# Performance work log

Measured on AMD Instinct MI355X. Metric: run time of the kernel, lower is better.

Reference implementation:

```python
import jax, jax.numpy as jnp
import numpy as np

T, B, E, H = 1024, 2, 1024, 16
D = E // H


def setup_inputs() -> dict:
    key = jax.random.key(0)
    ks = jax.random.split(key, 5)
    s = 1.0 / np.sqrt(E)  # xavier_uniform bound ~ sqrt(6/(fan_in+fan_out)); scale suffices for a numeric baseline
    return {
        "query": jax.random.normal(ks[0], (T, B, E), jnp.float32),
        "key_": jax.random.normal(ks[1], (T, B, E), jnp.float32),
        "value": jax.random.normal(ks[2], (T, B, E), jnp.float32),
        "in_proj_weight": jax.random.uniform(ks[3], (3 * E, E), jnp.float32, -s, s),
        "in_proj_bias": jnp.zeros((3 * E,), jnp.float32),
        "out_proj_weight": jax.random.uniform(ks[4], (E, E), jnp.float32, -s, s),
        "out_proj_bias": jnp.zeros((E,), jnp.float32),
    }


def reference(query, key_, value, in_proj_weight, in_proj_bias, out_proj_weight, out_proj_bias):
    # Faithful to CumulativeLinearMultiheadAttentionKV.forward with
    # batch_first=False, is_causal=True, no padding mask, no kv cache.
    Tl, Bl, El = query.shape
    wq, wk, wv = jnp.split(in_proj_weight, 3, axis=0)
    bq, bk, bv = jnp.split(in_proj_bias, 3)
    q = query @ wq.T + bq          # (T, B, E)
    k = key_ @ wk.T + bk
    v = value @ wv.T + bv

    def to_bhtd(x):
        return x.reshape(Tl, Bl, H, D).transpose(1, 2, 0, 3)  # (B, H, T, D)

    q, k, v = to_bhtd(q), to_bhtd(k), to_bhtd(v)

    scale = 1.0 / np.sqrt(D)  # SDPA-style default scale (scale=None)
    # cumulative linear attention: prefix sums of k_s \otimes v_s
    kv = jnp.einsum('bhsk,bhsv->bhskv', k, v)        # (B, H, T, D, D)
    kv_store = jnp.cumsum(kv, axis=2)                # causal KV state per step
    out = jnp.einsum('bhtk,bhtkv->bhtv', q, kv_store) * scale  # (B, H, T, D)

    out = out.transpose(2, 0, 1, 3).reshape(Tl, Bl, El)  # back to (T, B, E)
    out = out @ out_proj_weight.T + out_proj_bias
    return out
```

## Files before the change

kernel.cpp:

```cpp
#include <hip/hip_runtime.h>


#define T_SEQ 1024
#define B_SZ  2
#define E_DIM 1024
#define H_N   16
#define D_HD  64
#define NROWS (T_SEQ * B_SZ)
#define CHUNK 64
#define NCHUNK (T_SEQ / CHUNK)
#define BH (B_SZ * H_N)

typedef short bf16x8 __attribute__((ext_vector_type(8)));
typedef float f32x4  __attribute__((ext_vector_type(4)));

__device__ inline unsigned short f2bf(float f) {
    unsigned u = __builtin_bit_cast(unsigned, f);
    u = (u + 0x7FFFu + ((u >> 16) & 1u)) >> 16;
    return (unsigned short)u;
}

__device__ inline void gload_lds16(const void* g, void* l) {
    __builtin_amdgcn_global_load_lds(
        (const __attribute__((address_space(1))) unsigned int*)g,
        (__attribute__((address_space(3))) unsigned int*)l, 16, 0, 0);
}

__global__ __launch_bounds__(256) void k_castw(
    const float* __restrict__ w_in, const float* __restrict__ w_out,
    unsigned short* __restrict__ dst)
{
    const int id8 = blockIdx.x * 256 + threadIdx.x;
    const int WI8 = 3 * E_DIM * E_DIM / 8;
    const float* src = (id8 < WI8) ? (w_in + (size_t)id8 * 8)
                                   : (w_out + (size_t)(id8 - WI8) * 8);
    float4 f0 = *reinterpret_cast<const float4*>(src);
    float4 f1 = *reinterpret_cast<const float4*>(src + 4);
    ushort4 o0, o1;
    o0.x = f2bf(f0.x); o0.y = f2bf(f0.y); o0.z = f2bf(f0.z); o0.w = f2bf(f0.w);
    o1.x = f2bf(f1.x); o1.y = f2bf(f1.y); o1.z = f2bf(f1.z); o1.w = f2bf(f1.w);
    *reinterpret_cast<ushort4*>(dst + (size_t)id8 * 8)     = o0;
    *reinterpret_cast<ushort4*>(dst + (size_t)id8 * 8 + 4) = o1;
}

__global__ __launch_bounds__(256) void k_gin(
    const float* __restrict__ q_in, const float* __restrict__ k_in,
    const float* __restrict__ v_in, const unsigned short* __restrict__ Wibf,
    const float* __restrict__ b_in,
    unsigned short* __restrict__ qslab, unsigned short* __restrict__ kslab,
    unsigned short* __restrict__ ktb,   unsigned short* __restrict__ vtb)
{
    const int z = blockIdx.z;
    const float* X = (z == 0) ? q_in : (z == 1 ? k_in : v_in);
    const unsigned short* W = Wibf + (size_t)z * E_DIM * E_DIM;
    const float* bz = b_in + z * E_DIM;

    const int nBase = blockIdx.x * 128;
    const int mBase = blockIdx.y * 64;
    const int b = mBase >> 10;
    const int tBase = mBase & 1023;

    __shared__ short As[64 * 72];
    __shared__ short Bs[128 * 64];

    const int tid = threadIdx.x;
    const int lane = tid & 63, wave = tid >> 6;
    const int wr = wave >> 1, wc = wave & 1;
    const int l15 = lane & 15, l4 = lane >> 4;

    f32x4 acc[2][4] = {};

    for (int k0 = 0; k0 < E_DIM; k0 += 64) {
        #pragma unroll
        for (int l = 0; l < 4; ++l) {
            int off = l * 4096 + tid * 16;
            int row = off >> 7, kb = off & 127;
            gload_lds16((const char*)W + ((size_t)(nBase + row) * E_DIM + k0) * 2 + kb,
                        (char*)Bs + off);
        }
        #pragma unroll
        for (int l = 0; l < 2; ++l) {
            int u = tid + 256 * l;
            int row = u >> 3, ko = (u & 7) * 8;
            const float* src = &X[(size_t)((tBase + row) * 2 + b) * E_DIM + k0 + ko];
            float4 f0 = *reinterpret_cast<const float4*>(src);
            float4 f1 = *reinterpret_cast<const float4*>(src + 4);
            bf16x8 p;
            p[0] = (short)f2bf(f0.x); p[1] = (short)f2bf(f0.y);
            p[2] = (short)f2bf(f0.z); p[3] = (short)f2bf(f0.w);
            p[4] = (short)f2bf(f1.x); p[5] = (short)f2bf(f1.y);
            p[6] = (short)f2bf(f1.z); p[7] = (short)f2bf(f1.w);
            *reinterpret_cast<bf16x8*>(&As[row * 72 + ko]) = p;
        }
        __syncthreads();

        #pragma unroll
        for (int kk = 0; kk < 64; kk += 32) {
            bf16x8 af[2], bfr[4];
            #pragma unroll
            for (int i = 0; i < 2; ++i)
                af[i] = *reinterpret_cast<const bf16x8*>(
                            &As[(wr * 32 + i * 16 + l15) * 72 + kk + l4 * 8]);
            #pragma unroll
            for (int j = 0; j < 4; ++j)
                bfr[j] = *reinterpret_cast<const bf16x8*>(
                            &Bs[(wc * 64 + j * 16 + l15) * 64 + kk + l4 * 8]);
            #pragma unroll
            for (int i = 0; i < 2; ++i)
                #pragma unroll
                for (int j = 0; j < 4; ++j)
                    acc[i][j] = __builtin_amdgcn_mfma_f32_16x16x32_bf16(
                        af[i], bfr[j], acc[i][j], 0, 0, 0);
        }
        __syncthreads();
    }

    #pragma unroll
    for (int i = 0; i < 2; ++i) {
        int t0 = tBase + wr * 32 + i * 16 + l4 * 4;
        #pragma unroll
        for (int j = 0; j < 4; ++j) {
            int col = nBase + wc * 64 + j * 16 + l15;
            float bv = bz[col];
            unsigned short v4[4];
            #pragma unroll
            for (int q = 0; q < 4; ++q) v4[q] = f2bf(acc[i][j][q] + bv);
            if (z == 0) {
                #pragma unroll
                for (int q = 0; q < 4; ++q)
                    qslab[(size_t)b * 1048576 + (size_t)(t0 + q) * E_DIM + col] = v4[q];
            } else if (z == 1) {
                #pragma unroll
                for (int q = 0; q < 4; ++q)
                    kslab[(size_t)b * 1048576 + (size_t)(t0 + q) * E_DIM + col] = v4[q];
                ushort4 w = {v4[0], v4[1], v4[2], v4[3]};
                *reinterpret_cast<ushort4*>(
                    &ktb[((size_t)b * 1024 + col) * 1024 + t0]) = w;
            } else {
                ushort4 w = {v4[0], v4[1], v4[2], v4[3]};
                *reinterpret_cast<ushort4*>(
                    &vtb[((size_t)b * 1024 + col) * 1024 + t0]) = w;
            }
        }
    }
}

__global__ __launch_bounds__(256) void k_chunkkv(
    const unsigned short* __restrict__ ktb, const unsigned short* __restrict__ vtb,
    float* __restrict__ ckvT)
{
    const int c = blockIdx.x, bh = blockIdx.y;
    const int b = bh >> 4, h = bh & 15;
    const int colb = h * 64, t0 = c * CHUNK;

    __shared__ short Avs[64 * 64];
    __shared__ short Bks[64 * 64];

    const int tid = threadIdx.x;
    const int lane = tid & 63, wave = tid >> 6;
    const int wr = wave >> 1, wc = wave & 1;
    const int l15 = lane & 15, l4 = lane >> 4;

    #pragma unroll
    for (int l = 0; l < 2; ++l) {
        int off = l * 4096 + tid * 16;
        int row = off >> 7, kb = off & 127;
        size_t rbase = ((size_t)(b * 1024 + colb + row)) * 1024 + t0;
        gload_lds16((const char*)vtb + rbase * 2 + kb, (char*)Avs + off);
        gload_lds16((const char*)ktb + rbase * 2 + kb, (char*)Bks + off);
    }
    __syncthreads();

    f32x4 acc[2][2] = {};
    #pragma unroll
    for (int kk = 0; kk < 64; kk += 32) {
        bf16x8 af[2], bfr[2];
        #pragma unroll
        for (int i = 0; i < 2; ++i)
            af[i] = *reinterpret_cast<const bf16x8*>(
                        &Avs[(wr * 32 + i * 16 + l15) * 64 + kk + l4 * 8]);
        #pragma unroll
        for (int j = 0; j < 2; ++j)
            bfr[j] = *reinterpret_cast<const bf16x8*>(
                        &Bks[(wc * 32 + j * 16 + l15) * 64 + kk + l4 * 8]);
        #pragma unroll
        for (int i = 0; i < 2; ++i)
            #pragma unroll
            for (int j = 0; j < 2; ++j)
                acc[i][j] = __builtin_amdgcn_mfma_f32_16x16x32_bf16(
                    af[i], bfr[j], acc[i][j], 0, 0, 0);
    }

    float* dst = ckvT + ((size_t)bh * NCHUNK + c) * 4096;
    #pragma unroll
    for (int i = 0; i < 2; ++i) {
        int dv = wr * 32 + i * 16 + l4 * 4;
        #pragma unroll
        for (int j = 0; j < 2; ++j) {
            int dk = wc * 32 + j * 16 + l15;
            #pragma unroll
            for (int q = 0; q < 4; ++q)
                dst[(dv + q) * 64 + dk] = acc[i][j][q];
        }
    }
}

__global__ __launch_bounds__(256) void k_prefix(float* __restrict__ ckv)
{
    int id = blockIdx.x * blockDim.x + threadIdx.x;
    int bh = id >> 10, i4 = id & 1023;
    float4 run = {0.f, 0.f, 0.f, 0.f};
    float* base = ckv + (size_t)bh * NCHUNK * 4096 + (size_t)i4 * 4;
    for (int c = 0; c < NCHUNK; ++c) {
        float4* p = reinterpret_cast<float4*>(base + (size_t)c * 4096);
        float4 v = *p;
        *p = run;
        run.x += v.x; run.y += v.y; run.z += v.z; run.w += v.w;
    }
}

__global__ __launch_bounds__(256) void k_chunkout(
    const unsigned short* __restrict__ qslab, const unsigned short* __restrict__ kslab,
    const unsigned short* __restrict__ vtb,  const float* __restrict__ ckvT,
    unsigned short* __restrict__ attnbf)
{
    const int c = blockIdx.x, bh = blockIdx.y;
    const int b = bh >> 4, h = bh & 15;
    const int colb = h * 64, t0 = c * CHUNK;

    __shared__ short Qs[64 * 64];
    __shared__ short Ksn[64 * 64];
    __shared__ short Vts[64 * 64];
    __shared__ short PTs[64 * 72];
    __shared__ short Ss[64 * 72];

    const int tid = threadIdx.x;
    const int lane = tid & 63, wave = tid >> 6;
    const int wr = wave >> 1, wc = wave & 1;
    const int l15 = lane & 15, l4 = lane >> 4;

    #pragma unroll
    for (int l = 0; l < 2; ++l) {
        int off = l * 4096 + tid * 16;
        int row = off >> 7, kb = off & 127;
        size_t nat = ((size_t)b * 1048576 + (size_t)(t0 + row) * E_DIM + colb) * 2 + kb;
        gload_lds16((const char*)qslab + nat, (char*)Qs + off);
        gload_lds16((const char*)kslab + nat, (char*)Ksn + off);
        size_t trn = (((size_t)(b * 1024 + colb + row)) * 1024 + t0) * 2 + kb;
        gload_lds16((const char*)vtb + trn, (char*)Vts + off);
    }
    {
        const float* P = ckvT + ((size_t)bh * NCHUNK + c) * 4096;
        #pragma unroll
        for (int l = 0; l < 4; ++l) {
            int u = tid + 256 * l;
            int dv = u >> 4, dk4 = (u & 15) * 4;
            float4 f = *reinterpret_cast<const float4*>(&P[dv * 64 + dk4]);
            ushort4 w; w.x = f2bf(f.x); w.y = f2bf(f.y); w.z = f2bf(f.z); w.w = f2bf(f.w);
            *reinterpret_cast<ushort4*>(&PTs[dv * 72 + dk4]) = w;
        }
    }
    __syncthreads();

    f32x4 sacc[2][2] = {};
    #pragma unroll
    for (int kk = 0; kk < 64; kk += 32) {
        bf16x8 af[2], bfr[2];
        #pragma unroll
        for (int i = 0; i < 2; ++i)
            af[i] = *reinterpret_cast<const bf16x8*>(
                        &Qs[(wr * 32 + i * 16 + l15) * 64 + kk + l4 * 8]);
        #pragma unroll
        for (int j = 0; j < 2; ++j)
            bfr[j] = *reinterpret_cast<const bf16x8*>(
                        &Ksn[(wc * 32 + j * 16 + l15) * 64 + kk + l4 * 8]);
        #pragma unroll
        for (int i = 0; i < 2; ++i)
            #pragma unroll
            for (int j = 0; j < 2; ++j)
                sacc[i][j] = __builtin_amdgcn_mfma_f32_16x16x32_bf16(
                    af[i], bfr[j], sacc[i][j], 0, 0, 0);
    }
    #pragma unroll
    for (int i = 0; i < 2; ++i) {
        int qr = wr * 32 + i * 16 + l4 * 4;
        #pragma unroll
        for (int j = 0; j < 2; ++j) {
            int kr = wc * 32 + j * 16 + l15;
            #pragma unroll
            for (int q = 0; q < 4; ++q)
                Ss[(qr + q) * 72 + kr] =
                    (kr <= qr + q) ? (short)f2bf(sacc[i][j][q]) : (short)0;
        }
    }
    __syncthreads();

    f32x4 oacc[2][2] = {};
    #pragma unroll
    for (int kk = 0; kk < 64; kk += 32) {
        bf16x8 af[2], bfr[2];
        #pragma unroll
        for (int i = 0; i < 2; ++i)
            af[i] = *reinterpret_cast<const bf16x8*>(
                        &Ss[(wr * 32 + i * 16 + l15) * 72 + kk + l4 * 8]);
        #pragma unroll
        for (int j = 0; j < 2; ++j)
            bfr[j] = *reinterpret_cast<const bf16x8*>(
                        &Vts[(wc * 32 + j * 16 + l15) * 64 + kk + l4 * 8]);
        #pragma unroll
        for (int i = 0; i < 2; ++i)
            #pragma unroll
            for (int j = 0; j < 2; ++j)
                oacc[i][j] = __builtin_amdgcn_mfma_f32_16x16x32_bf16(
                    af[i], bfr[j], oacc[i][j], 0, 0, 0);
    }
    #pragma unroll
    for (int kk = 0; kk < 64; kk += 32) {
        bf16x8 af[2], bfr[2];
        #pragma unroll
        for (int i = 0; i < 2; ++i)
            af[i] = *reinterpret_cast<const bf16x8*>(
                        &Qs[(wr * 32 + i * 16 + l15) * 64 + kk + l4 * 8]);
        #pragma unroll
        for (int j = 0; j < 2; ++j)
            bfr[j] = *reinterpret_cast<const bf16x8*>(
                        &PTs[(wc * 32 + j * 16 + l15) * 72 + kk + l4 * 8]);
        #pragma unroll
        for (int i = 0; i < 2; ++i)
            #pragma unroll
            for (int j = 0; j < 2; ++j)
                oacc[i][j] = __builtin_amdgcn_mfma_f32_16x16x32_bf16(
                    af[i], bfr[j], oacc[i][j], 0, 0, 0);
    }

    #pragma unroll
    for (int i = 0; i < 2; ++i) {
        int qr = wr * 32 + i * 16 + l4 * 4;
        #pragma unroll
        for (int j = 0; j < 2; ++j) {
            int dv = wc * 32 + j * 16 + l15;
            #pragma unroll
            for (int q = 0; q < 4; ++q)
                attnbf[(size_t)b * 1048576 + (size_t)(t0 + qr + q) * E_DIM + colb + dv] =
                    f2bf(oacc[i][j][q] * 0.125f);
        }
    }
}

__global__ __launch_bounds__(256) void k_gout(
    const unsigned short* __restrict__ attnbf, const unsigned short* __restrict__ Wobf,
    const float* __restrict__ bias, float* __restrict__ out)
{
    const int nBase = blockIdx.x * 128;
    const int mBase = blockIdx.y * 64;

    __shared__ short As[64 * 64];
    __shared__ short Bs[128 * 64];

    const int tid = threadIdx.x;
    const int lane = tid & 63, wave = tid >> 6;
    const int wr = wave >> 1, wc = wave & 1;
    const int l15 = lane & 15, l4 = lane >> 4;

    f32x4 acc[2][4] = {};

    for (int k0 = 0; k0 < E_DIM; k0 += 64) {
        #pragma unroll
        for (int l = 0; l < 4; ++l) {
            int off = l * 4096 + tid * 16;
            int row = off >> 7, kb = off & 127;
            gload_lds16((const char*)Wobf + ((size_t)(nBase + row) * E_DIM + k0) * 2 + kb,
                        (char*)Bs + off);
        }
        #pragma unroll
        for (int l = 0; l < 2; ++l) {
            int off = l * 4096 + tid * 16;
            int row = off >> 7, kb = off & 127;
            int r = mBase + row, t = r >> 1, bb = r & 1;
            gload_lds16((const char*)attnbf +
                            ((size_t)bb * 1048576 + (size_t)t * E_DIM + k0) * 2 + kb,
                        (char*)As + off);
        }
        __syncthreads();

        #pragma unroll
        for (int kk = 0; kk < 64; kk += 32) {
            bf16x8 af[2], bfr[4];
            #pragma unroll
            for (int i = 0; i < 2; ++i)
                af[i] = *reinterpret_cast<const bf16x8*>(
                            &As[(wr * 32 + i * 16 + l15) * 64 + kk + l4 * 8]);
            #pragma unroll
            for (int j = 0; j < 4; ++j)
                bfr[j] = *reinterpret_cast<const bf16x8*>(
                            &Bs[(wc * 64 + j * 16 + l15) * 64 + kk + l4 * 8]);
            #pragma unroll
            for (int i = 0; i < 2; ++i)
                #pragma unroll
                for (int j = 0; j < 4; ++j)
                    acc[i][j] = __builtin_amdgcn_mfma_f32_16x16x32_bf16(
                        af[i], bfr[j], acc[i][j], 0, 0, 0);
        }
        __syncthreads();
    }

    #pragma unroll
    for (int i = 0; i < 2; ++i) {
        int r0 = mBase + wr * 32 + i * 16 + l4 * 4;
        #pragma unroll
        for (int j = 0; j < 4; ++j) {
            int col = nBase + wc * 64 + j * 16 + l15;
            float bv = bias[col];
            #pragma unroll
            for (int q = 0; q < 4; ++q)
                out[(size_t)(r0 + q) * E_DIM + col] = acc[i][j][q] + bv;
        }
    }
}

extern "C" void kernel_launch(void* const* d_in, const int* in_sizes, int n_in,
                              void* d_out, int out_size, void* d_ws, size_t ws_size,
                              hipStream_t stream)
{
    const float* q_in  = (const float*)d_in[0];
    const float* k_in  = (const float*)d_in[1];
    const float* v_in  = (const float*)d_in[2];
    const float* w_in  = (const float*)d_in[3];
    const float* b_in  = (const float*)d_in[4];
    const float* w_out = (const float*)d_in[5];
    const float* b_out = (const float*)d_in[6];

    char* w = (char*)d_ws;
    unsigned short* Wibf   = (unsigned short*)w;
    unsigned short* Wobf   = (unsigned short*)(w + 6291456);
    unsigned short* qslab  = (unsigned short*)(w + 8388608);
    unsigned short* kslab  = (unsigned short*)(w + 12582912);
    unsigned short* ktb    = (unsigned short*)(w + 16777216);
    unsigned short* vtb    = (unsigned short*)(w + 20971520);
    float*          ckvT   = (float*)(w + 25165824);
    unsigned short* attnbf = (unsigned short*)(w + 33554432);
    float* outp = (float*)d_out;

    k_castw<<<2048, 256, 0, stream>>>(w_in, w_out, Wibf);

    k_gin<<<dim3(8, 32, 3), 256, 0, stream>>>(
        q_in, k_in, v_in, Wibf, b_in, qslab, kslab, ktb, vtb);

    k_chunkkv<<<dim3(NCHUNK, BH), 256, 0, stream>>>(ktb, vtb, ckvT);
    k_prefix<<<dim3(BH * 1024 / 256), 256, 0, stream>>>(ckvT);
    k_chunkout<<<dim3(NCHUNK, BH), 256, 0, stream>>>(qslab, kslab, vtb, ckvT, attnbf);

    k_gout<<<dim3(8, 32), 256, 0, stream>>>(attnbf, Wobf, b_out, outp);
}
```

Measured before the change: 155.4 us.

## Replace chunked KV-state attention with quadratic masked QK^T V and pre-cast inputs

The chunked linear-attention pipeline (per-chunk K^T V states, a prefix-sum kernel, and chunk output) is replaced by a single kernel. For each 64-row query tile it loops over all earlier key chunks, computing a causally masked QK^T and multiplying by V. Activations are now cast to bf16 together with the weights in one combined cast kernel, so the input GEMM loads bf16 tiles directly into LDS asynchronously. The GEMM and attention grids are remapped for XCD locality, and attention uses a zigzag tile order for load balance. This drops the fp32 KV-state traffic and two launches, but adds quadratic work and per-chunk syncs, and the extra cast pass writes 12MB of bf16 activations.

Result: no change. 156.5 us (+0.7%).

```diff
diff --git a/kernel.cpp b/kernel.cpp
--- a/kernel.cpp
+++ b/kernel.cpp
@@ -1,15 +1,7 @@
 #include <hip/hip_runtime.h>
 
 
-#define T_SEQ 1024
-#define B_SZ  2
 #define E_DIM 1024
-#define H_N   16
-#define D_HD  64
-#define NROWS (T_SEQ * B_SZ)
-#define CHUNK 64
-#define NCHUNK (T_SEQ / CHUNK)
-#define BH (B_SZ * H_N)
 
 typedef short bf16x8 __attribute__((ext_vector_type(8)));
 typedef float f32x4  __attribute__((ext_vector_type(4)));
@@ -26,41 +18,49 @@
         (__attribute__((address_space(3))) unsigned int*)l, 16, 0, 0);
 }
 
-__global__ __launch_bounds__(256) void k_castw(
-    const float* __restrict__ w_in, const float* __restrict__ w_out,
-    unsigned short* __restrict__ dst)
-{
-    const int id8 = blockIdx.x * 256 + threadIdx.x;
-    const int WI8 = 3 * E_DIM * E_DIM / 8;
-    const float* src = (id8 < WI8) ? (w_in + (size_t)id8 * 8)
-                                   : (w_out + (size_t)(id8 - WI8) * 8);
-    float4 f0 = *reinterpret_cast<const float4*>(src);
-    float4 f1 = *reinterpret_cast<const float4*>(src + 4);
-    ushort4 o0, o1;
-    o0.x = f2bf(f0.x); o0.y = f2bf(f0.y); o0.z = f2bf(f0.z); o0.w = f2bf(f0.w);
-    o1.x = f2bf(f1.x); o1.y = f2bf(f1.y); o1.z = f2bf(f1.z); o1.w = f2bf(f1.w);
-    *reinterpret_cast<ushort4*>(dst + (size_t)id8 * 8)     = o0;
-    *reinterpret_cast<ushort4*>(dst + (size_t)id8 * 8 + 4) = o1;
+__global__ __launch_bounds__(256) void k_cast(
+    const float* __restrict__ q_in, const float* __restrict__ k_in,
+    const float* __restrict__ v_in, const float* __restrict__ w_in,
+    const float* __restrict__ w_out, unsigned short* __restrict__ dst)
+{
+    #pragma unroll
+    for (int l = 0; l < 4; ++l) {
+        int id8 = blockIdx.x * 256 + threadIdx.x + l * 327680;
+        const float* src;
+        if (id8 < 262144)        src = q_in  + (size_t)id8 * 8;
+        else if (id8 < 524288)   src = k_in  + (size_t)(id8 - 262144) * 8;
+        else if (id8 < 786432)   src = v_in  + (size_t)(id8 - 524288) * 8;
+        else if (id8 < 1179648)  src = w_in  + (size_t)(id8 - 786432) * 8;
+        else                     src = w_out + (size_t)(id8 - 1179648) * 8;
+        float4 f0 = *reinterpret_cast<const float4*>(src);
+        float4 f1 = *reinterpret_cast<const float4*>(src + 4);
+        ushort4 o0, o1;
+        o0.x = f2bf(f0.x); o0.y = f2bf(f0.y); o0.z = f2bf(f0.z); o0.w = f2bf(f0.w);
+        o1.x = f2bf(f1.x); o1.y = f2bf(f1.y); o1.z = f2bf(f1.z); o1.w = f2bf(f1.w);
+        *reinterpret_cast<ushort4*>(dst + (size_t)id8 * 8)     = o0;
+        *reinterpret_cast<ushort4*>(dst + (size_t)id8 * 8 + 4) = o1;
+    }
 }
 
 __global__ __launch_bounds__(256) void k_gin(
-    const float* __restrict__ q_in, const float* __restrict__ k_in,
-    const float* __restrict__ v_in, const unsigned short* __restrict__ Wibf,
+    const unsigned short* __restrict__ xbf, const unsigned short* __restrict__ Wibf,
     const float* __restrict__ b_in,
     unsigned short* __restrict__ qslab, unsigned short* __restrict__ kslab,
-    unsigned short* __restrict__ ktb,   unsigned short* __restrict__ vtb)
-{
-    const int z = blockIdx.z;
-    const float* X = (z == 0) ? q_in : (z == 1 ? k_in : v_in);
-    const unsigned short* W = Wibf + (size_t)z * E_DIM * E_DIM;
+    unsigned short* __restrict__ vtb)
+{
+    const int i = blockIdx.x;
+    const int tile = (i & 7) * 96 + (i >> 3);
+    const int x = tile & 7, y = (tile >> 3) & 31, z = tile >> 8;
+
+    const unsigned short* X = xbf + (size_t)z * 2097152;
+    const unsigned short* W = Wibf + (size_t)z * 1048576;
     const float* bz = b_in + z * E_DIM;
 
-    const int nBase = blockIdx.x * 128;
-    const int mBase = blockIdx.y * 64;
-    const int b = mBase >> 10;
-    const int tBase = mBase & 1023;
-
-    __shared__ short As[64 * 72];
+    const int nBase = x * 128;
+    const int mBase = y * 64;
+    const int b = mBase >> 10, tBase = mBase & 1023;
+
+    __shared__ short As[64 * 64];
     __shared__ short Bs[128 * 64];
 
     const int tid = threadIdx.x;
@@ -80,17 +80,11 @@
         }
         #pragma unroll
         for (int l = 0; l < 2; ++l) {
-            int u = tid + 256 * l;
-            int row = u >> 3, ko = (u & 7) * 8;
-            const float* src = &X[(size_t)((tBase + row) * 2 + b) * E_DIM + k0 + ko];
-            float4 f0 = *reinterpret_cast<const float4*>(src);
-            float4 f1 = *reinterpret_cast<const float4*>(src + 4);
-            bf16x8 p;
-            p[0] = (short)f2bf(f0.x); p[1] = (short)f2bf(f0.y);
-            p[2] = (short)f2bf(f0.z); p[3] = (short)f2bf(f0.w);
-            p[4] = (short)f2bf(f1.x); p[5] = (short)f2bf(f1.y);
-            p[6] = (short)f2bf(f1.z); p[7] = (short)f2bf(f1.w);
-            *reinterpret_cast<bf16x8*>(&As[row * 72 + ko]) = p;
+            int off = l * 4096 + tid * 16;
+            int row = off >> 7, kb = off & 127;
+            gload_lds16((const char*)X +
+                            ((size_t)((tBase + row) * 2 + b) * E_DIM + k0) * 2 + kb,
+                        (char*)As + off);
         }
         __syncthreads();
 
@@ -98,33 +92,33 @@
         for (int kk = 0; kk < 64; kk += 32) {
             bf16x8 af[2], bfr[4];
             #pragma unroll
-            for (int i = 0; i < 2; ++i)
-                af[i] = *reinterpret_cast<const bf16x8*>(
-                            &As[(wr * 32 + i * 16 + l15) * 72 + kk + l4 * 8]);
+            for (int ii = 0; ii < 2; ++ii)
+                af[ii] = *reinterpret_cast<const bf16x8*>(
+                            &As[(wr * 32 + ii * 16 + l15) * 64 + kk + l4 * 8]);
             #pragma unroll
             for (int j = 0; j < 4; ++j)
                 bfr[j] = *reinterpret_cast<const bf16x8*>(
                             &Bs[(wc * 64 + j * 16 + l15) * 64 + kk + l4 * 8]);
             #pragma unroll
-            for (int i = 0; i < 2; ++i)
+            for (int ii = 0; ii < 2; ++ii)
                 #pragma unroll
                 for (int j = 0; j < 4; ++j)
-                    acc[i][j] = __builtin_amdgcn_mfma_f32_16x16x32_bf16(
-                        af[i], bfr[j], acc[i][j], 0, 0, 0);
-        }
-        __syncthreads();
-    }
-
-    #pragma unroll
-    for (int i = 0; i < 2; ++i) {
-        int t0 = tBase + wr * 32 + i * 16 + l4 * 4;
+                    acc[ii][j] = __builtin_amdgcn_mfma_f32_16x16x32_bf16(
+                        af[ii], bfr[j], acc[ii][j], 0, 0, 0);
+        }
+        __syncthreads();
+    }
+
+    #pragma unroll
+    for (int ii = 0; ii < 2; ++ii) {
+        int t0 = tBase + wr * 32 + ii * 16 + l4 * 4;
         #pragma unroll
         for (int j = 0; j < 4; ++j) {
             int col = nBase + wc * 64 + j * 16 + l15;
             float bv = bz[col];
             unsigned short v4[4];
             #pragma unroll
-            for (int q = 0; q < 4; ++q) v4[q] = f2bf(acc[i][j][q] + bv);
+            for (int q = 0; q < 4; ++q) v4[q] = f2bf(acc[ii][j][q] + bv);
             if (z == 0) {
                 #pragma unroll
                 for (int q = 0; q < 4; ++q)
@@ -133,9 +127,6 @@
                 #pragma unroll
                 for (int q = 0; q < 4; ++q)
                     kslab[(size_t)b * 1048576 + (size_t)(t0 + q) * E_DIM + col] = v4[q];
-                ushort4 w = {v4[0], v4[1], v4[2], v4[3]};
-                *reinterpret_cast<ushort4*>(
-                    &ktb[((size_t)b * 1024 + col) * 1024 + t0]) = w;
             } else {
                 ushort4 w = {v4[0], v4[1], v4[2], v4[3]};
                 *reinterpret_cast<ushort4*>(
@@ -145,16 +136,22 @@
     }
 }
 
-__global__ __launch_bounds__(256) void k_chunkkv(
-    const unsigned short* __restrict__ ktb, const unsigned short* __restrict__ vtb,
-    float* __restrict__ ckvT)
-{
-    const int c = blockIdx.x, bh = blockIdx.y;
+__global__ __launch_bounds__(256) void k_attn(
+    const unsigned short* __restrict__ qslab, const unsigned short* __restrict__ kslab,
+    const unsigned short* __restrict__ vtb, unsigned short* __restrict__ attnbf)
+{
+    const int i = blockIdx.x;
+    const int xcd = i & 7, u = i >> 3;
+    const int bh = xcd * 4 + (u >> 4);
+    const int qtr = u & 15;
+    const int qt = ((u >> 5) & 1) ? (15 - qtr) : qtr;
     const int b = bh >> 4, h = bh & 15;
-    const int colb = h * 64, t0 = c * CHUNK;
-
-    __shared__ short Avs[64 * 64];
-    __shared__ short Bks[64 * 64];
+    const int colb = h * 64, t0q = qt * 64;
+
+    __shared__ short Qs[64 * 64];
+    __shared__ short Ks[64 * 64];
+    __shared__ short Vts[64 * 64];
+    __shared__ short Ss[64 * 72];
 
     const int tid = threadIdx.x;
     const int lane = tid & 63, wave = tid >> 6;
@@ -165,203 +162,117 @@
     for (int l = 0; l < 2; ++l) {
         int off = l * 4096 + tid * 16;
         int row = off >> 7, kb = off & 127;
-        size_t rbase = ((size_t)(b * 1024 + colb + row)) * 1024 + t0;
-        gload_lds16((const char*)vtb + rbase * 2 + kb, (char*)Avs + off);
-        gload_lds16((const char*)ktb + rbase * 2 + kb, (char*)Bks + off);
-    }
-    __syncthreads();
-
-    f32x4 acc[2][2] = {};
-    #pragma unroll
-    for (int kk = 0; kk < 64; kk += 32) {
-        bf16x8 af[2], bfr[2];
-        #pragma unroll
-        for (int i = 0; i < 2; ++i)
-            af[i] = *reinterpret_cast<const bf16x8*>(
-                        &Avs[(wr * 32 + i * 16 + l15) * 64 + kk + l4 * 8]);
-        #pragma unroll
-        for (int j = 0; j < 2; ++j)
-            bfr[j] = *reinterpret_cast<const bf16x8*>(
-                        &Bks[(wc * 32 + j * 16 + l15) * 64 + kk + l4 * 8]);
-        #pragma unroll
-        for (int i = 0; i < 2; ++i)
+        gload_lds16((const char*)qslab +
+                        ((size_t)b * 1048576 + (size_t)(t0q + row) * E_DIM + colb) * 2 + kb,
+                    (char*)Qs + off);
+    }
+
+    f32x4 oacc[2][2] = {};
+
+    for (int c = 0; c <= qt; ++c) {
+        const int t0k = c * 64;
+        #pragma unroll
+        for (int l = 0; l < 2; ++l) {
+            int off = l * 4096 + tid * 16;
+            int row = off >> 7, kb = off & 127;
+            gload_lds16((const char*)kslab +
+                            ((size_t)b * 1048576 + (size_t)(t0k + row) * E_DIM + colb) * 2 + kb,
+                        (char*)Ks + off);
+            gload_lds16((const char*)vtb +
+                            (((size_t)b * 1024 + colb + row) * 1024 + t0k) * 2 + kb,
+                        (char*)Vts + off);
+        }
+        __syncthreads();
+
+        f32x4 sacc[2][2] = {};
+        #pragma unroll
+        for (int kk = 0; kk < 64; kk += 32) {
+            bf16x8 af[2], bfr[2];
+            #pragma unroll
+            for (int ii = 0; ii < 2; ++ii)
+                af[ii] = *reinterpret_cast<const bf16x8*>(
+                            &Qs[(wr * 32 + ii * 16 + l15) * 64 + kk + l4 * 8]);
             #pragma unroll
             for (int j = 0; j < 2; ++j)
-                acc[i][j] = __builtin_amdgcn_mfma_f32_16x16x32_bf16(
-                    af[i], bfr[j], acc[i][j], 0, 0, 0);
-    }
-
-    float* dst = ckvT + ((size_t)bh * NCHUNK + c) * 4096;
-    #pragma unroll
-    for (int i = 0; i < 2; ++i) {
-        int dv = wr * 32 + i * 16 + l4 * 4;
+                bfr[j] = *reinterpret_cast<const bf16x8*>(
+                            &Ks[(wc * 32 + j * 16 + l15) * 64 + kk + l4 * 8]);
+            #pragma unroll
+            for (int ii = 0; ii < 2; ++ii)
+                #pragma unroll
+                for (int j = 0; j < 2; ++j)
+                    sacc[ii][j] = __builtin_amdgcn_mfma_f32_16x16x32_bf16(
+                        af[ii], bfr[j], sacc[ii][j], 0, 0, 0);
+        }
+        const bool diag = (c == qt);
+        #pragma unroll
+        for (int ii = 0; ii < 2; ++ii) {
+            #pragma unroll
+            for (int j = 0; j < 2; ++j) {
+                int kr = wc * 32 + j * 16 + l15;
+                #pragma unroll
+                for (int q = 0; q < 4; ++q) {
+                    int qr = wr * 32 + ii * 16 + l4 * 4 + q;
+                    short sv = (short)f2bf(sacc[ii][j][q]);
+                    Ss[qr * 72 + kr] = (!diag || kr <= qr) ? sv : (short)0;
+                }
+            }
+        }
+        __syncthreads();
+
+        #pragma unroll
+        for (int kk = 0; kk < 64; kk += 32) {
+            bf16x8 af[2], bfr[2];
+            #pragma unroll
+            for (int ii = 0; ii < 2; ++ii)
+                af[ii] = *reinterpret_cast<const bf16x8*>(
+                            &Ss[(wr * 32 + ii * 16 + l15) * 72 + kk + l4 * 8]);
+            #pragma unroll
+            for (int j = 0; j < 2; ++j)
+                bfr[j] = *reinterpret_cast<const bf16x8*>(
+                            &Vts[(wc * 32 + j * 16 + l15) * 64 + kk + l4 * 8]);
+            #pragma unroll
+            for (int ii = 0; ii < 2; ++ii)
+                #pragma unroll
+                for (int j = 0; j < 2; ++j)
+                    oacc[ii][j] = __builtin_amdgcn_mfma_f32_16x16x32_bf16(
+                        af[ii], bfr[j], oacc[ii][j], 0, 0, 0);
+        }
+        __syncthreads();
+    }
+
+    #pragma unroll
+    for (int ii = 0; ii < 2; ++ii) {
         #pragma unroll
         for (int j = 0; j < 2; ++j) {
-            int dk = wc * 32 + j * 16 + l15;
-            #pragma unroll
-            for (int q = 0; q < 4; ++q)
-                dst[(dv + q) * 64 + dk] = acc[i][j][q];
-        }
-    }
-}
-
-__global__ __launch_bounds__(256) void k_prefix(float* __restrict__ ckv)
-{
-    int id = blockIdx.x * blockDim.x + threadIdx.x;
-    int bh = id >> 10, i4 = id & 1023;
-    float4 run = {0.f, 0.f, 0.f, 0.f};
-    float* base = ckv + (size_t)bh * NCHUNK * 4096 + (size_t)i4 * 4;
-    for (int c = 0; c < NCHUNK; ++c) {
-        float4* p = reinterpret_cast<float4*>(base + (size_t)c * 4096);
-        float4 v = *p;
-        *p = run;
-        run.x += v.x; run.y += v.y; run.z += v.z; run.w += v.w;
-    }
-}
-
-__global__ __launch_bounds__(256) void k_chunkout(
-    const unsigned short* __restrict__ qslab, const unsigned short* __restrict__ kslab,
-    const unsigned short* __restrict__ vtb,  const float* __restrict__ ckvT,
-    unsigned short* __restrict__ attnbf)
-{
-    const int c = blockIdx.x, bh = blockIdx.y;
-    const int b = bh >> 4, h = bh & 15;
-    const int colb = h * 64, t0 = c * CHUNK;
-
-    __shared__ short Qs[64 * 64];
-    __shared__ short Ksn[64 * 64];
-    __shared__ short Vts[64 * 64];
-    __shared__ short PTs[64 * 72];
-    __shared__ short Ss[64 * 72];
+            int dv = wc * 32 + j * 16 + l15;
+            #pragma unroll
+            for (int q = 0; q < 4; ++q) {
+                int qr = wr * 32 + ii * 16 + l4 * 4 + q;
+                attnbf[(size_t)b * 1048576 + (size_t)(t0q + qr) * E_DIM + colb + dv] =
+                    f2bf(oacc[ii][j][q] * 0.125f);
+            }
+        }
+    }
+}
+
+__global__ __launch_bounds__(256) void k_gout(
+    const unsigned short* __restrict__ attnbf, const unsigned short* __restrict__ Wobf,
+    const float* __restrict__ bias, float* __restrict__ out)
+{
+    const int i = blockIdx.x;
+    const int tile = (i & 7) * 32 + (i >> 3);
+    const int x = tile & 7, y = tile >> 3;
+    const int nBase = x * 128;
+    const int mBase = y * 64;
+
+    __shared__ short As[64 * 64];
+    __shared__ short Bs[128 * 64];
 
     const int tid = threadIdx.x;
     const int lane = tid & 63, wave = tid >> 6;
     const int wr = wave >> 1, wc = wave & 1;
     const int l15 = lane & 15, l4 = lane >> 4;
 
-    #pragma unroll
-    for (int l = 0; l < 2; ++l) {
-        int off = l * 4096 + tid * 16;
-        int row = off >> 7, kb = off & 127;
-        size_t nat = ((size_t)b * 1048576 + (size_t)(t0 + row) * E_DIM + colb) * 2 + kb;
-        gload_lds16((const char*)qslab + nat, (char*)Qs + off);
-        gload_lds16((const char*)kslab + nat, (char*)Ksn + off);
-        size_t trn = (((size_t)(b * 1024 + colb + row)) * 1024 + t0) * 2 + kb;
-        gload_lds16((const char*)vtb + trn, (char*)Vts + off);
-    }
-    {
-        const float* P = ckvT + ((size_t)bh * NCHUNK + c) * 4096;
-        #pragma unroll
-        for (int l = 0; l < 4; ++l) {
-            int u = tid + 256 * l;
-            int dv = u >> 4, dk4 = (u & 15) * 4;
-            float4 f = *reinterpret_cast<const float4*>(&P[dv * 64 + dk4]);
-            ushort4 w; w.x = f2bf(f.x); w.y = f2bf(f.y); w.z = f2bf(f.z); w.w = f2bf(f.w);
-            *reinterpret_cast<ushort4*>(&PTs[dv * 72 + dk4]) = w;
-        }
-    }
-    __syncthreads();
-
-    f32x4 sacc[2][2] = {};
-    #pragma unroll
-    for (int kk = 0; kk < 64; kk += 32) {
-        bf16x8 af[2], bfr[2];
-        #pragma unroll
-        for (int i = 0; i < 2; ++i)
-            af[i] = *reinterpret_cast<const bf16x8*>(
-                        &Qs[(wr * 32 + i * 16 + l15) * 64 + kk + l4 * 8]);
-        #pragma unroll
-        for (int j = 0; j < 2; ++j)
-            bfr[j] = *reinterpret_cast<const bf16x8*>(
-                        &Ksn[(wc * 32 + j * 16 + l15) * 64 + kk + l4 * 8]);
-        #pragma unroll
-        for (int i = 0; i < 2; ++i)
-            #pragma unroll
-            for (int j = 0; j < 2; ++j)
-                sacc[i][j] = __builtin_amdgcn_mfma_f32_16x16x32_bf16(
-                    af[i], bfr[j], sacc[i][j], 0, 0, 0);
-    }
-    #pragma unroll
-    for (int i = 0; i < 2; ++i) {
-        int qr = wr * 32 + i * 16 + l4 * 4;
-        #pragma unroll
-        for (int j = 0; j < 2; ++j) {
-            int kr = wc * 32 + j * 16 + l15;
-            #pragma unroll
-            for (int q = 0; q < 4; ++q)
-                Ss[(qr + q) * 72 + kr] =
-                    (kr <= qr + q) ? (short)f2bf(sacc[i][j][q]) : (short)0;
-        }
-    }
-    __syncthreads();
-
-    f32x4 oacc[2][2] = {};
-    #pragma unroll
-    for (int kk = 0; kk < 64; kk += 32) {
-        bf16x8 af[2], bfr[2];
-        #pragma unroll
-        for (int i = 0; i < 2; ++i)
-            af[i] = *reinterpret_cast<const bf16x8*>(
-                        &Ss[(wr * 32 + i * 16 + l15) * 72 + kk + l4 * 8]);
-        #pragma unroll
-        for (int j = 0; j < 2; ++j)
-            bfr[j] = *reinterpret_cast<const bf16x8*>(
-                        &Vts[(wc * 32 + j * 16 + l15) * 64 + kk + l4 * 8]);
-        #pragma unroll
-        for (int i = 0; i < 2; ++i)
-            #pragma unroll
-            for (int j = 0; j < 2; ++j)
-                oacc[i][j] = __builtin_amdgcn_mfma_f32_16x16x32_bf16(
-                    af[i], bfr[j], oacc[i][j], 0, 0, 0);
-    }
-    #pragma unroll
-    for (int kk = 0; kk < 64; kk += 32) {
-        bf16x8 af[2], bfr[2];
-        #pragma unroll
-        for (int i = 0; i < 2; ++i)
-            af[i] = *reinterpret_cast<const bf16x8*>(
-                        &Qs[(wr * 32 + i * 16 + l15) * 64 + kk + l4 * 8]);
-        #pragma unroll
-        for (int j = 0; j < 2; ++j)
-            bfr[j] = *reinterpret_cast<const bf16x8*>(
-                        &PTs[(wc * 32 + j * 16 + l15) * 72 + kk + l4 * 8]);
-        #pragma unroll
-        for (int i = 0; i < 2; ++i)
-            #pragma unroll
-            for (int j = 0; j < 2; ++j)
-                oacc[i][j] = __builtin_amdgcn_mfma_f32_16x16x32_bf16(
-                    af[i], bfr[j], oacc[i][j], 0, 0, 0);
-    }
-
-    #pragma unroll
-    for (int i = 0; i < 2; ++i) {
-        int qr = wr * 32 + i * 16 + l4 * 4;
-        #pragma unroll
-        for (int j = 0; j < 2; ++j) {
-            int dv = wc * 32 + j * 16 + l15;
-            #pragma unroll
-            for (int q = 0; q < 4; ++q)
-                attnbf[(size_t)b * 1048576 + (size_t)(t0 + qr + q) * E_DIM + colb + dv] =
-                    f2bf(oacc[i][j][q] * 0.125f);
-        }
-    }
-}
-
-__global__ __launch_bounds__(256) void k_gout(
-    const unsigned short* __restrict__ attnbf, const unsigned short* __restrict__ Wobf,
-    const float* __restrict__ bias, float* __restrict__ out)
-{
-    const int nBase = blockIdx.x * 128;
-    const int mBase = blockIdx.y * 64;
-
-    __shared__ short As[64 * 64];
-    __shared__ short Bs[128 * 64];
-
-    const int tid = threadIdx.x;
-    const int lane = tid & 63, wave = tid >> 6;
-    const int wr = wave >> 1, wc = wave & 1;
-    const int l15 = lane & 15, l4 = lane >> 4;
-
     f32x4 acc[2][4] = {};
 
     for (int k0 = 0; k0 < E_DIM; k0 += 64) {
@@ -387,33 +298,33 @@
         for (int kk = 0; kk < 64; kk += 32) {
             bf16x8 af[2], bfr[4];
             #pragma unroll
-            for (int i = 0; i < 2; ++i)
-                af[i] = *reinterpret_cast<const bf16x8*>(
-                            &As[(wr * 32 + i * 16 + l15) * 64 + kk + l4 * 8]);
+            for (int ii = 0; ii < 2; ++ii)
+                af[ii] = *reinterpret_cast<const bf16x8*>(
+                            &As[(wr * 32 + ii * 16 + l15) * 64 + kk + l4 * 8]);
             #pragma unroll
             for (int j = 0; j < 4; ++j)
                 bfr[j] = *reinterpret_cast<const bf16x8*>(
                             &Bs[(wc * 64 + j * 16 + l15) * 64 + kk + l4 * 8]);
             #pragma unroll
-            for (int i = 0; i < 2; ++i)
+            for (int ii = 0; ii < 2; ++ii)
                 #pragma unroll
                 for (int j = 0; j < 4; ++j)
-                    acc[i][j] = __builtin_amdgcn_mfma_f32_16x16x32_bf16(
-                        af[i], bfr[j], acc[i][j], 0, 0, 0);
-        }
-        __syncthreads();
-    }
-
-    #pragma unroll
-    for (int i = 0; i < 2; ++i) {
-        int r0 = mBase + wr * 32 + i * 16 + l4 * 4;
+                    acc[ii][j] = __builtin_amdgcn_mfma_f32_16x16x32_bf16(
+                        af[ii], bfr[j], acc[ii][j], 0, 0, 0);
+        }
+        __syncthreads();
+    }
+
+    #pragma unroll
+    for (int ii = 0; ii < 2; ++ii) {
+        int r0 = mBase + wr * 32 + ii * 16 + l4 * 4;
         #pragma unroll
         for (int j = 0; j < 4; ++j) {
             int col = nBase + wc * 64 + j * 16 + l15;
             float bv = bias[col];
             #pragma unroll
             for (int q = 0; q < 4; ++q)
-                out[(size_t)(r0 + q) * E_DIM + col] = acc[i][j][q] + bv;
+                out[(size_t)(r0 + q) * E_DIM + col] = acc[ii][j][q] + bv;
         }
     }
 }
@@ -431,24 +342,17 @@
     const float* b_out = (const float*)d_in[6];
 
     char* w = (char*)d_ws;
-    unsigned short* Wibf   = (unsigned short*)w;
-    unsigned short* Wobf   = (unsigned short*)(w + 6291456);
-    unsigned short* qslab  = (unsigned short*)(w + 8388608);
-    unsigned short* kslab  = (unsigned short*)(w + 12582912);
-    unsigned short* ktb    = (unsigned short*)(w + 16777216);
-    unsigned short* vtb    = (unsigned short*)(w + 20971520);
-    float*          ckvT   = (float*)(w + 25165824);
+    unsigned short* xbf    = (unsigned short*)w;
+    unsigned short* Wibf   = (unsigned short*)(w + 12582912);
+    unsigned short* Wobf   = (unsigned short*)(w + 18874368);
+    unsigned short* qslab  = (unsigned short*)(w + 20971520);
+    unsigned short* kslab  = (unsigned short*)(w + 25165824);
+    unsigned short* vtb    = (unsigned short*)(w + 29360128);
     unsigned short* attnbf = (unsigned short*)(w + 33554432);
     float* outp = (float*)d_out;
 
-    k_castw<<<2048, 256, 0, stream>>>(w_in, w_out, Wibf);
-
-    k_gin<<<dim3(8, 32, 3), 256, 0, stream>>>(
-        q_in, k_in, v_in, Wibf, b_in, qslab, kslab, ktb, vtb);
-
-    k_chunkkv<<<dim3(NCHUNK, BH), 256, 0, stream>>>(ktb, vtb, ckvT);
-    k_prefix<<<dim3(BH * 1024 / 256), 256, 0, stream>>>(ckvT);
-    k_chunkout<<<dim3(NCHUNK, BH), 256, 0, stream>>>(qslab, kslab, vtb, ckvT, attnbf);
-
-    k_gout<<<dim3(8, 32), 256, 0, stream>>>(attnbf, Wobf, b_out, outp);
-}
+    k_cast<<<1280, 256, 0, stream>>>(q_in, k_in, v_in, w_in, w_out, xbf);
+    k_gin<<<768, 256, 0, stream>>>(xbf, Wibf, b_in, qslab, kslab, vtb);
+    k_attn<<<512, 256, 0, stream>>>(qslab, kslab, vtb, attnbf);
+    k_gout<<<256, 256, 0, stream>>>(attnbf, Wobf, b_out, outp);
+}
```
